# Kernel optimization log

Measured on AMD Instinct MI355X. Metric: run time of the kernel, lower is better.

## Reference

```python
import jax, jax.numpy as jnp
import numpy as np

B, N, DIM = 4, 2048, 512
H, DH = 8, 64  # n_heads, dim_head; inner = H*DH = 512
SCALE = DH ** -0.5


def setup_inputs() -> dict:
    key = jax.random.key(0)
    k1, k2, k3 = jax.random.split(key, 3)
    inner = H * DH
    X = jax.random.normal(k1, (B, N, DIM), dtype=jnp.float32)
    W_qkv = jax.random.normal(k2, (DIM, 3 * inner), dtype=jnp.float32) * (DIM ** -0.5)
    W_out = jax.random.normal(k3, (inner, DIM), dtype=jnp.float32) * (inner ** -0.5)
    b_out = jnp.zeros((DIM,), dtype=jnp.float32)
    return {"X": X, "W_qkv": W_qkv, "W_out": W_out, "b_out": b_out}


def reference(X, W_qkv, W_out, b_out):
    # X: (b, n, dim)
    qkv = X @ W_qkv                      # (b, n, 3*h*d)
    q, k, v = jnp.split(qkv, 3, axis=-1)
    def to_heads(t):
        b, n, _ = t.shape
        return t.reshape(b, n, H, DH).transpose(0, 2, 1, 3)  # (b, h, n, d)
    q, k, v = to_heads(q), to_heads(k), to_heads(v)
    # NOTE: original computes scores[n, m] = k_n . q_m and softmaxes over m (query axis)
    scores = jnp.einsum('bhnd,bhmd->bhnm', k, q) * SCALE     # (b, h, n_k, m_q)
    att = jax.nn.softmax(scores, axis=-1)
    # out token axis is the KEY index n: out[n, d] = sum_e att[n, e] * v[e, d]
    out = jnp.einsum('bhne,bhed->bhnd', att, v)              # (b, h, n, d)
    out = out.transpose(0, 2, 1, 3).reshape(X.shape[0], X.shape[1], H * DH)  # (b, n, h*d)
    return out @ W_out + b_out
```

## Files before the change

kernel.cpp:

```cpp
#include <hip/hip_runtime.h>
#include <hip/hip_bf16.h>

typedef __bf16 bf16_t;
typedef bf16_t bf16x8 __attribute__((ext_vector_type(8)));
typedef bf16_t bf16x4v __attribute__((ext_vector_type(4)));
typedef float f32x4 __attribute__((ext_vector_type(4)));

#define B_SZ 4
#define N_TOK 2048
#define DIM 512
#define H_N 8
#define DH 64
#define INNER 512
#define M_ROWS 8192
#define NQKV 1536
#define K_FOLD 0.18033688011112042f

#define GLD_LDS16(gp, lp)                                          \
  __builtin_amdgcn_global_load_lds(                                \
      (const __attribute__((address_space(1))) void*)(gp),         \
      (__attribute__((address_space(3))) void*)(lp), 16, 0, 0)

__device__ __forceinline__ float fexp2(float x) {
#if __has_builtin(__builtin_amdgcn_exp2f)
  return __builtin_amdgcn_exp2f(x);
#else
  float r;
  asm volatile("v_exp_f32 %0, %1\n\ts_nop 1" : "=v"(r) : "v"(x));
  return r;
#endif
}


__global__ void f32_to_bf16_kernel(const float* __restrict__ src,
                                   bf16_t* __restrict__ dst, int n4) {
  int i = blockIdx.x * blockDim.x + threadIdx.x;
  int stride = gridDim.x * blockDim.x;
  for (; i < n4; i += stride) {
    float4 f = reinterpret_cast<const float4*>(src)[i];
    bf16x4v o;
    o.x = (bf16_t)f.x; o.y = (bf16_t)f.y; o.z = (bf16_t)f.z; o.w = (bf16_t)f.w;
    reinterpret_cast<bf16x4v*>(dst)[i] = o;
  }
}

__global__ void transpose_f32_to_bf16_kernel(const float* __restrict__ src,
                                             bf16_t* __restrict__ dst, int R, int C) {
  int t = blockIdx.x * blockDim.x + threadIdx.x;
  if (t >= R * C) return;
  int r = t / C, c = t - r * C;
  dst[(size_t)c * R + r] = (bf16_t)src[t];
}

template <int MODE>
__global__ __launch_bounds__(256) void gemm_bf16_kernel(
    const bf16_t* __restrict__ A, const bf16_t* __restrict__ Bt,
    int M, int Nn, int K,
    bf16_t* __restrict__ qb, bf16_t* __restrict__ kb, bf16_t* __restrict__ vtb,
    float* __restrict__ outF, const float* __restrict__ bias) {
  __shared__ bf16_t As[128 * 64];
  __shared__ bf16_t Bs[128 * 64];

  const int tid = threadIdx.x;
  const int lane = tid & 63;
  const int wave = tid >> 6;
  const int g = lane >> 4, c = lane & 15;
  const int wm = (wave >> 1) * 64, wn = (wave & 1) * 64;
  const int m0 = blockIdx.x * 128, n0 = blockIdx.y * 128;

  f32x4 acc[4][4] = {};

  for (int k0 = 0; k0 < K; k0 += 64) {
    __syncthreads();
    #pragma unroll
    for (int i = 0; i < 4; ++i) {
      int blk = i * 256 + tid;
      int row = blk >> 3;
      int cb = (blk & 7) ^ (row & 7);
      int base = (i * 256 + wave * 64) * 8;
      GLD_LDS16(A + (size_t)(m0 + row) * K + k0 + cb * 8, &As[base]);
      GLD_LDS16(Bt + (size_t)(n0 + row) * K + k0 + cb * 8, &Bs[base]);
    }
    __syncthreads();
    __builtin_amdgcn_s_setprio(1);
    #pragma unroll
    for (int ks = 0; ks < 2; ++ks) {
      bf16x8 af[4], bfr[4];
      #pragma unroll
      for (int i = 0; i < 4; ++i) {
        af[i] = *reinterpret_cast<const bf16x8*>(
            &As[(wm + i * 16 + c) * 64 + (((ks * 4 + g) ^ (c & 7)) * 8)]);
        bfr[i] = *reinterpret_cast<const bf16x8*>(
            &Bs[(wn + i * 16 + c) * 64 + (((ks * 4 + g) ^ (c & 7)) * 8)]);
      }
      #pragma unroll
      for (int mi = 0; mi < 4; ++mi)
        #pragma unroll
        for (int ni = 0; ni < 4; ++ni)
          acc[mi][ni] = __builtin_amdgcn_mfma_f32_16x16x32_bf16(
              af[mi], bfr[ni], acc[mi][ni], 0, 0, 0);
    }
    __builtin_amdgcn_s_setprio(0);
  }

  #pragma unroll
  for (int mi = 0; mi < 4; ++mi) {
    #pragma unroll
    for (int ni = 0; ni < 4; ++ni) {
      int colg = n0 + wn + ni * 16 + c;
      if (MODE == 0) {
        int s = colg >> 9;
        int hh = (colg >> 6) & 7, dd = colg & 63;
        int rowg0 = m0 + wm + mi * 16 + g * 4;
        int bb = rowg0 >> 11, nn = rowg0 & 2047;
        if (s == 2) {
          bf16x4v pk;
          pk.x = (bf16_t)acc[mi][ni][0];
          pk.y = (bf16_t)acc[mi][ni][1];
          pk.z = (bf16_t)acc[mi][ni][2];
          pk.w = (bf16_t)acc[mi][ni][3];
          *reinterpret_cast<bf16x4v*>(
              &vtb[(((size_t)(bb * H_N + hh)) * DH + dd) * N_TOK + nn]) = pk;
        } else {
          float sc = (s == 1) ? K_FOLD : 1.0f;
          bf16_t* dst = (s == 0) ? qb : kb;
          #pragma unroll
          for (int r = 0; r < 4; ++r)
            dst[(((size_t)(bb * H_N + hh)) * N_TOK + nn + r) * DH + dd] =
                (bf16_t)(acc[mi][ni][r] * sc);
        }
      } else {
        #pragma unroll
        for (int r = 0; r < 4; ++r) {
          int rowg = m0 + wm + mi * 16 + g * 4 + r;
          outF[(size_t)rowg * Nn + colg] = acc[mi][ni][r] + bias[colg];
        }
      }
    }
  }
}

__global__ __launch_bounds__(512, 4) void attn_kernel(
    const bf16_t* __restrict__ Qproj, const bf16_t* __restrict__ Kproj,
    const bf16_t* __restrict__ Vt, bf16_t* __restrict__ att_out) {
  const int glin = blockIdx.x;
  const int xcd = glin & 7;
  const int j = glin >> 3;
  const int hb = xcd * 4 + (j >> 4);
  const int rb = j & 15;
  const int h = hb & 7, b = hb >> 3;

  const size_t hbo = (size_t)(b * H_N + h);
  const bf16_t* Aq = Kproj + hbo * N_TOK * DH;
  const bf16_t* Ak = Qproj + hbo * N_TOK * DH;
  const bf16_t* Av = Vt + hbo * (size_t)DH * N_TOK;

  const int tid = threadIdx.x, lane = tid & 63, wave = tid >> 6;
  const int g = lane >> 4, c = lane & 15;
  const int r0 = rb * 128, wr0 = wave * 16;

  __shared__ bf16_t sK[2][64 * 64];
  __shared__ bf16_t sV[3][64 * 64];
  __shared__ bf16_t sP[8][2][16 * 72];

  bf16x8 qreg[2];
  #pragma unroll
  for (int ks = 0; ks < 2; ++ks)
    qreg[ks] = *reinterpret_cast<const bf16x8*>(
        &Aq[(size_t)(r0 + wr0 + c) * DH + ks * 32 + g * 8]);

  f32x4 accO[4] = {};
  float Lp[4] = {0.f, 0.f, 0.f, 0.f};

  const int srow = tid >> 3;
  const int scb = (tid & 7) ^ (srow & 7);

  auto stageK = [&](int buf, int j0) {
    GLD_LDS16(Ak + (size_t)(j0 + srow) * DH + scb * 8, &sK[buf][wave * 512]);
  };
  auto stageV = [&](int buf, int j0) {
    GLD_LDS16(Av + (size_t)srow * N_TOK + j0 + scb * 8, &sV[buf][wave * 512]);
  };

  stageK(0, 0);
  stageV(0, 0);
  __syncthreads();

  constexpr int NT = N_TOK / 64;
  int vcur = 0, vold = 0;
  for (int t = 0; t < NT; ++t) {
    int vnext = (vcur == 2) ? 0 : vcur + 1;
    if (t + 1 < NT) {
      stageK((t + 1) & 1, (t + 1) * 64);
      stageV(vnext, (t + 1) * 64);
    }
    const bf16_t* bK = sK[t & 1];

    __builtin_amdgcn_s_setprio(1);
    f32x4 accT[4] = {};
    #pragma unroll
    for (int ks = 0; ks < 2; ++ks) {
      bf16x8 ak[4];
      #pragma unroll
      for (int mi = 0; mi < 4; ++mi)
        ak[mi] = *reinterpret_cast<const bf16x8*>(
            &bK[(mi * 16 + c) * 64 + (((ks * 4 + g) ^ (c & 7)) * 8)]);
      #pragma unroll
      for (int mi = 0; mi < 4; ++mi)
        accT[mi] = __builtin_amdgcn_mfma_f32_16x16x32_bf16(
            ak[mi], qreg[ks], accT[mi], 0, 0, 0);
    }

    if (t > 0) {
      const bf16_t* bV = sV[vold];
      const bf16_t* pp = sP[wave][(t & 1) ^ 1];
      #pragma unroll
      for (int ks = 0; ks < 2; ++ks) {
        bf16x8 pa = *reinterpret_cast<const bf16x8*>(&pp[c * 72 + ks * 32 + g * 8]);
        #pragma unroll
        for (int di = 0; di < 4; ++di) {
          bf16x8 vv = *reinterpret_cast<const bf16x8*>(
              &bV[(di * 16 + c) * 64 + (((ks * 4 + g) ^ (c & 7)) * 8)]);
          accO[di] = __builtin_amdgcn_mfma_f32_16x16x32_bf16(pa, vv, accO[di], 0, 0, 0);
        }
      }
    }
    __builtin_amdgcn_s_setprio(0);

    bf16_t* pw = sP[wave][t & 1];
    #pragma unroll
    for (int mi = 0; mi < 4; ++mi) {
      float p0 = fexp2(accT[mi][0]);
      float p1 = fexp2(accT[mi][1]);
      float p2 = fexp2(accT[mi][2]);
      float p3 = fexp2(accT[mi][3]);
      Lp[mi] += (p0 + p1) + (p2 + p3);
      bf16x4v pk;
      pk.x = (bf16_t)p0; pk.y = (bf16_t)p1; pk.z = (bf16_t)p2; pk.w = (bf16_t)p3;
      *reinterpret_cast<bf16x4v*>(&pw[c * 72 + mi * 16 + g * 4]) = pk;
    }

    __syncthreads();
    vold = vcur;
    vcur = vnext;
  }

  {
    const bf16_t* bV = sV[vold];
    const bf16_t* pp = sP[wave][(NT - 1) & 1];
    #pragma unroll
    for (int ks = 0; ks < 2; ++ks) {
      bf16x8 pa = *reinterpret_cast<const bf16x8*>(&pp[c * 72 + ks * 32 + g * 8]);
      #pragma unroll
      for (int di = 0; di < 4; ++di) {
        bf16x8 vv = *reinterpret_cast<const bf16x8*>(
            &bV[(di * 16 + c) * 64 + (((ks * 4 + g) ^ (c & 7)) * 8)]);
        accO[di] = __builtin_amdgcn_mfma_f32_16x16x32_bf16(pa, vv, accO[di], 0, 0, 0);
      }
    }
  }

  float l = (Lp[0] + Lp[1]) + (Lp[2] + Lp[3]);
  l += __shfl_xor(l, 16);
  l += __shfl_xor(l, 32);
  float invL = 1.0f / l;
  #pragma unroll
  for (int r = 0; r < 4; ++r) {
    float inv = __shfl(invL, g * 4 + r);
    int row = r0 + wr0 + g * 4 + r;
    #pragma unroll
    for (int di = 0; di < 4; ++di) {
      int col = h * DH + di * 16 + c;
      att_out[((size_t)(b * N_TOK) + row) * INNER + col] =
          (bf16_t)(accO[di][r] * inv);
    }
  }
}


extern "C" void kernel_launch(void* const* d_in, const int* in_sizes, int n_in,
                              void* d_out, int out_size, void* d_ws, size_t ws_size,
                              hipStream_t stream) {
  const float* X    = (const float*)d_in[0];
  const float* Wqkv = (const float*)d_in[1];
  const float* Wout = (const float*)d_in[2];
  const float* bout = (const float*)d_in[3];
  float* out = (float*)d_out;

  char* ws = (char*)d_ws;
  bf16_t* Xb    = (bf16_t*)(ws);
  bf16_t* WqkvT = (bf16_t*)(ws + 8388608);
  bf16_t* WoutT = (bf16_t*)(ws + 9961472);
  bf16_t* Qb    = (bf16_t*)(ws + 10485760);
  bf16_t* Kb    = (bf16_t*)(ws + 18874368);
  bf16_t* Vtb   = (bf16_t*)(ws + 27262976);
  bf16_t* AttO  = (bf16_t*)(ws + 35651584);

  f32_to_bf16_kernel<<<2048, 256, 0, stream>>>(X, Xb, (M_ROWS * DIM) / 4);
  transpose_f32_to_bf16_kernel<<<(DIM * NQKV + 255) / 256, 256, 0, stream>>>(
      Wqkv, WqkvT, DIM, NQKV);
  transpose_f32_to_bf16_kernel<<<(INNER * DIM + 255) / 256, 256, 0, stream>>>(
      Wout, WoutT, INNER, DIM);

  dim3 g1(M_ROWS / 128, NQKV / 128);
  gemm_bf16_kernel<0><<<g1, 256, 0, stream>>>(Xb, WqkvT, M_ROWS, NQKV, DIM,
                                              Qb, Kb, Vtb, nullptr, nullptr);

  attn_kernel<<<dim3(512), 512, 0, stream>>>(Qb, Kb, Vtb, AttO);

  dim3 g3(M_ROWS / 128, DIM / 128);
  gemm_bf16_kernel<1><<<g3, 256, 0, stream>>>(AttO, WoutT, M_ROWS, DIM, DIM,
                                              nullptr, nullptr, nullptr, out, bout);
}
```

Before: 94.08 us.

## Rewrite attention inner loop with 32x32x16 MFMA and four-wave blocks

```diff
diff --git a/kernel.cpp b/kernel.cpp
--- a/kernel.cpp
+++ b/kernel.cpp
@@ -5,6 +5,7 @@
 typedef bf16_t bf16x8 __attribute__((ext_vector_type(8)));
 typedef bf16_t bf16x4v __attribute__((ext_vector_type(4)));
 typedef float f32x4 __attribute__((ext_vector_type(4)));
+typedef float f32x16 __attribute__((ext_vector_type(16)));
 
 #define B_SZ 4
 #define N_TOK 2048
@@ -140,14 +141,14 @@
   }
 }
 
-__global__ __launch_bounds__(512, 4) void attn_kernel(
+__global__ __launch_bounds__(256, 2) void attn_kernel(
     const bf16_t* __restrict__ Qproj, const bf16_t* __restrict__ Kproj,
     const bf16_t* __restrict__ Vt, bf16_t* __restrict__ att_out) {
   const int glin = blockIdx.x;
   const int xcd = glin & 7;
-  const int j = glin >> 3;
-  const int hb = xcd * 4 + (j >> 4);
-  const int rb = j & 15;
+  const int jj = glin >> 3;
+  const int hb = xcd * 4 + (jj >> 4);
+  const int rb = jj & 15;
   const int h = hb & 7, b = hb >> 3;
 
   const size_t hbo = (size_t)(b * H_N + h);
@@ -156,123 +157,107 @@
   const bf16_t* Av = Vt + hbo * (size_t)DH * N_TOK;
 
   const int tid = threadIdx.x, lane = tid & 63, wave = tid >> 6;
-  const int g = lane >> 4, c = lane & 15;
-  const int r0 = rb * 128, wr0 = wave * 16;
+  const int nl = lane & 31;
+  const int hf = lane >> 5;
+  const int r0 = rb * 128, wr0 = wave * 32;
+  const int rot = ((lane >> 3) & 3) * 16;
 
   __shared__ bf16_t sK[2][64 * 64];
-  __shared__ bf16_t sV[3][64 * 64];
-  __shared__ bf16_t sP[8][2][16 * 72];
-
-  bf16x8 qreg[2];
+  __shared__ bf16_t sV[2][64 * 64];
+  __shared__ bf16_t sP[4][32 * 72];
+
+  bf16x8 qreg[4];
   #pragma unroll
-  for (int ks = 0; ks < 2; ++ks)
+  for (int ks = 0; ks < 4; ++ks)
     qreg[ks] = *reinterpret_cast<const bf16x8*>(
-        &Aq[(size_t)(r0 + wr0 + c) * DH + ks * 32 + g * 8]);
-
-  f32x4 accO[4] = {};
-  float Lp[4] = {0.f, 0.f, 0.f, 0.f};
-
-  const int srow = tid >> 3;
-  const int scb = (tid & 7) ^ (srow & 7);
-
-  auto stageK = [&](int buf, int j0) {
-    GLD_LDS16(Ak + (size_t)(j0 + srow) * DH + scb * 8, &sK[buf][wave * 512]);
+        &Aq[(size_t)(r0 + wr0 + nl) * DH + ks * 16 + hf * 8]);
+
+  f32x16 accO[2] = {};
+  float Lp[2] = {0.f, 0.f};
+
+  auto stage = [&](bf16_t* dK, bf16_t* dV, int j0) {
+    #pragma unroll
+    for (int i = 0; i < 2; ++i) {
+      int blk = i * 256 + tid;
+      int row = blk >> 3;
+      int cb = (blk & 7) ^ (row & 7);
+      int base = (i * 256 + wave * 64) * 8;
+      GLD_LDS16(Ak + (size_t)(j0 + row) * DH + cb * 8, dK + base);
+      GLD_LDS16(Av + (size_t)row * N_TOK + j0 + cb * 8, dV + base);
+    }
   };
-  auto stageV = [&](int buf, int j0) {
-    GLD_LDS16(Av + (size_t)srow * N_TOK + j0 + scb * 8, &sV[buf][wave * 512]);
-  };
-
-  stageK(0, 0);
-  stageV(0, 0);
+
+  stage(sK[0], sV[0], 0);
   __syncthreads();
 
   constexpr int NT = N_TOK / 64;
-  int vcur = 0, vold = 0;
   for (int t = 0; t < NT; ++t) {
-    int vnext = (vcur == 2) ? 0 : vcur + 1;
-    if (t + 1 < NT) {
-      stageK((t + 1) & 1, (t + 1) * 64);
-      stageV(vnext, (t + 1) * 64);
-    }
+    if (t + 1 < NT) stage(sK[(t + 1) & 1], sV[(t + 1) & 1], (t + 1) * 64);
     const bf16_t* bK = sK[t & 1];
-
+    const bf16_t* bV = sV[t & 1];
+
+    f32x16 accT[2] = {};
     __builtin_amdgcn_s_setprio(1);
-    f32x4 accT[4] = {};
-    #pragma unroll
-    for (int ks = 0; ks < 2; ++ks) {
-      bf16x8 ak[4];
+    #pragma unroll
+    for (int ks = 0; ks < 4; ++ks) {
+      bf16x8 ak0 = *reinterpret_cast<const bf16x8*>(
+          &bK[nl * 64 + (((ks * 2 + hf) ^ (nl & 7)) * 8)]);
+      bf16x8 ak1 = *reinterpret_cast<const bf16x8*>(
+          &bK[(32 + nl) * 64 + (((ks * 2 + hf) ^ (nl & 7)) * 8)]);
+      accT[0] = __builtin_amdgcn_mfma_f32_32x32x16_bf16(ak0, qreg[ks], accT[0], 0, 0, 0);
+      accT[1] = __builtin_amdgcn_mfma_f32_32x32x16_bf16(ak1, qreg[ks], accT[1], 0, 0, 0);
+    }
+    __builtin_amdgcn_s_setprio(0);
+
+    #pragma unroll
+    for (int mi = 0; mi < 2; ++mi) {
       #pragma unroll
-      for (int mi = 0; mi < 4; ++mi)
-        ak[mi] = *reinterpret_cast<const bf16x8*>(
-            &bK[(mi * 16 + c) * 64 + (((ks * 4 + g) ^ (c & 7)) * 8)]);
-      #pragma unroll
-      for (int mi = 0; mi < 4; ++mi)
-        accT[mi] = __builtin_amdgcn_mfma_f32_16x16x32_bf16(
-            ak[mi], qreg[ks], accT[mi], 0, 0, 0);
-    }
-
-    if (t > 0) {
-      const bf16_t* bV = sV[vold];
-      const bf16_t* pp = sP[wave][(t & 1) ^ 1];
-      #pragma unroll
-      for (int ks = 0; ks < 2; ++ks) {
-        bf16x8 pa = *reinterpret_cast<const bf16x8*>(&pp[c * 72 + ks * 32 + g * 8]);
-        #pragma unroll
-        for (int di = 0; di < 4; ++di) {
-          bf16x8 vv = *reinterpret_cast<const bf16x8*>(
-              &bV[(di * 16 + c) * 64 + (((ks * 4 + g) ^ (c & 7)) * 8)]);
-          accO[di] = __builtin_amdgcn_mfma_f32_16x16x32_bf16(pa, vv, accO[di], 0, 0, 0);
-        }
+      for (int q = 0; q < 4; ++q) {
+        float p0 = fexp2(accT[mi][4 * q + 0]);
+        float p1 = fexp2(accT[mi][4 * q + 1]);
+        float p2 = fexp2(accT[mi][4 * q + 2]);
+        float p3 = fexp2(accT[mi][4 * q + 3]);
+        Lp[mi] += (p0 + p1) + (p2 + p3);
+        bf16x4v pk;
+        pk.x = (bf16_t)p0; pk.y = (bf16_t)p1; pk.z = (bf16_t)p2; pk.w = (bf16_t)p3;
+        int M = mi * 32 + 8 * q + 4 * hf;
+        *reinterpret_cast<bf16x4v*>(&sP[wave][nl * 72 + ((M + rot) & 63)]) = pk;
       }
     }
+
+    __builtin_amdgcn_s_setprio(1);
+    #pragma unroll
+    for (int ks = 0; ks < 4; ++ks) {
+      bf16x8 pfrag = *reinterpret_cast<const bf16x8*>(
+          &sP[wave][nl * 72 + ((ks * 16 + hf * 8 + rot) & 63)]);
+      bf16x8 av0 = *reinterpret_cast<const bf16x8*>(
+          &bV[nl * 64 + (((ks * 2 + hf) ^ (nl & 7)) * 8)]);
+      bf16x8 av1 = *reinterpret_cast<const bf16x8*>(
+          &bV[(32 + nl) * 64 + (((ks * 2 + hf) ^ (nl & 7)) * 8)]);
+      accO[0] = __builtin_amdgcn_mfma_f32_32x32x16_bf16(av0, pfrag, accO[0], 0, 0, 0);
+      accO[1] = __builtin_amdgcn_mfma_f32_32x32x16_bf16(av1, pfrag, accO[1], 0, 0, 0);
+    }
     __builtin_amdgcn_s_setprio(0);
 
-    bf16_t* pw = sP[wave][t & 1];
-    #pragma unroll
-    for (int mi = 0; mi < 4; ++mi) {
-      float p0 = fexp2(accT[mi][0]);
-      float p1 = fexp2(accT[mi][1]);
-      float p2 = fexp2(accT[mi][2]);
-      float p3 = fexp2(accT[mi][3]);
-      Lp[mi] += (p0 + p1) + (p2 + p3);
-      bf16x4v pk;
-      pk.x = (bf16_t)p0; pk.y = (bf16_t)p1; pk.z = (bf16_t)p2; pk.w = (bf16_t)p3;
-      *reinterpret_cast<bf16x4v*>(&pw[c * 72 + mi * 16 + g * 4]) = pk;
-    }
-
     __syncthreads();
-    vold = vcur;
-    vcur = vnext;
-  }
-
-  {
-    const bf16_t* bV = sV[vold];
-    const bf16_t* pp = sP[wave][(NT - 1) & 1];
-    #pragma unroll
-    for (int ks = 0; ks < 2; ++ks) {
-      bf16x8 pa = *reinterpret_cast<const bf16x8*>(&pp[c * 72 + ks * 32 + g * 8]);
-      #pragma unroll
-      for (int di = 0; di < 4; ++di) {
-        bf16x8 vv = *reinterpret_cast<const bf16x8*>(
-            &bV[(di * 16 + c) * 64 + (((ks * 4 + g) ^ (c & 7)) * 8)]);
-        accO[di] = __builtin_amdgcn_mfma_f32_16x16x32_bf16(pa, vv, accO[di], 0, 0, 0);
-      }
-    }
-  }
-
-  float l = (Lp[0] + Lp[1]) + (Lp[2] + Lp[3]);
-  l += __shfl_xor(l, 16);
+  }
+
+  float l = Lp[0] + Lp[1];
   l += __shfl_xor(l, 32);
   float invL = 1.0f / l;
+  const int nrow = r0 + wr0 + nl;
   #pragma unroll
-  for (int r = 0; r < 4; ++r) {
-    float inv = __shfl(invL, g * 4 + r);
-    int row = r0 + wr0 + g * 4 + r;
-    #pragma unroll
-    for (int di = 0; di < 4; ++di) {
-      int col = h * DH + di * 16 + c;
-      att_out[((size_t)(b * N_TOK) + row) * INNER + col] =
-          (bf16_t)(accO[di][r] * inv);
+  for (int di = 0; di < 2; ++di) {
+    #pragma unroll
+    for (int q = 0; q < 4; ++q) {
+      int d0 = 32 * di + 8 * q + 4 * hf;
+      bf16x4v o;
+      o.x = (bf16_t)(accO[di][4 * q + 0] * invL);
+      o.y = (bf16_t)(accO[di][4 * q + 1] * invL);
+      o.z = (bf16_t)(accO[di][4 * q + 2] * invL);
+      o.w = (bf16_t)(accO[di][4 * q + 3] * invL);
+      *reinterpret_cast<bf16x4v*>(
+          &att_out[((size_t)(b * N_TOK) + nrow) * INNER + h * DH + d0]) = o;
     }
   }
 }
@@ -306,7 +291,7 @@
   gemm_bf16_kernel<0><<<g1, 256, 0, stream>>>(Xb, WqkvT, M_ROWS, NQKV, DIM,
                                               Qb, Kb, Vtb, nullptr, nullptr);
 
-  attn_kernel<<<dim3(512), 512, 0, stream>>>(Qb, Kb, Vtb, AttO);
+  attn_kernel<<<dim3(512), 256, 0, stream>>>(Qb, Kb, Vtb, AttO);
 
   dim3 g3(M_ROWS / 128, DIM / 128);
   gemm_bf16_kernel<1><<<g3, 256, 0, stream>>>(AttO, WoutT, M_ROWS, DIM, DIM,
```

Result: slower. 96.90 us (+3.0%).
